# Kernel tuning notes

Measured on AMD Instinct MI355X. Metric: run time of the kernel, lower is better.

The kernel has to match this reference:

```python
import jax, jax.numpy as jnp
import numpy as np

# Dims: B INRs, N probe points, d_in=2 coords, hidden H, out D_OUT, proj P
B, N, D_IN, H, D_OUT, P = 128, 4096, 2, 128, 3, 128
W0_SIREN = 30.0  # SIREN frequency scale
LN_EPS = 1e-5


def setup_inputs() -> dict:
    key = jax.random.key(0)
    ks = jax.random.split(key, 12)
    sn = lambda k, shape, sc: (jax.random.normal(k, shape, dtype=jnp.float32) * sc)
    return {
        # per-sample SIREN params, torch layout: weight [b, in, out, 1], bias [b, out, 1]
        "w0": sn(ks[0], (B, D_IN, H, 1), 1.0 / D_IN),
        "w1": sn(ks[1], (B, H, H, 1), np.sqrt(6.0 / H) / W0_SIREN),
        "w2": sn(ks[2], (B, H, D_OUT, 1), np.sqrt(6.0 / H) / W0_SIREN),
        "b0": sn(ks[3], (B, H, 1), 0.1),
        "b1": sn(ks[4], (B, H, 1), 0.1),
        "b2": sn(ks[5], (B, D_OUT, 1), 0.1),
        # learned probe coordinates, initialized U[-1, 1) as in the module
        "inputs": jax.random.uniform(ks[6], (1, N, D_IN), dtype=jnp.float32, minval=-1.0, maxval=1.0),
        # projection (num_inputs -> proj_dim) + LayerNorm params, one per probed layer (4 total)
        "pw": sn(ks[7], (4, N, P), 1.0 / np.sqrt(N)),
        "pb": jnp.zeros((4, P), jnp.float32),
        "ln_g": jnp.ones((4, P), jnp.float32),
        "ln_b": jnp.zeros((4, P), jnp.float32),
    }


def _layernorm(x, g, b):
    m = jnp.mean(x, axis=-1, keepdims=True)
    v = jnp.mean(jnp.square(x - m), axis=-1, keepdims=True)
    return (x - m) * jax.lax.rsqrt(v + LN_EPS) * g + b


def reference(w0, w1, w2, b0, b1, b2, inputs, pw, pb, ln_g, ln_b):
    b = w0.shape[0]
    x = jnp.broadcast_to(inputs, (b,) + inputs.shape[1:])  # [b, n, d_in]

    def lin(h, W, bb):
        # per-sample linear: [b,n,i] @ [b,i,o] + [b,1,o]
        return jnp.einsum('bni,bio->bno', h, W[..., 0]) + bb[:, None, :, 0]

    h1 = jnp.sin(W0_SIREN * lin(x, w0, b0))   # [b, n, H]
    h2 = jnp.sin(W0_SIREN * lin(h1, w1, b1))  # [b, n, H]
    h3 = lin(h2, w2, b2)                      # [b, n, D_OUT] (last layer: no sine)
    feats = [x, h1, h2, h3]  # probe features per node layer (input coords + activations)

    outs = []
    for i, f in enumerate(feats):
        # permute to [b, dim_i, n], project n -> P, then LayerNorm over P
        z = jnp.einsum('bnd,np->bdp', f, pw[i]) + pb[i]
        outs.append(_layernorm(z, ln_g[i], ln_b[i]))
    return jnp.concatenate(outs, axis=1)  # [b, d_in + H + H + D_OUT, P]
```

## Files before the change

### kernel.cpp

```cpp
#include <hip/hip_runtime.h>
#include <hip/hip_bf16.h>


typedef unsigned short u16;
typedef __attribute__((ext_vector_type(8))) short short8;
typedef __attribute__((ext_vector_type(4))) short short4v;
typedef __attribute__((ext_vector_type(4))) float f32x4;
typedef __attribute__((ext_vector_type(4))) float float4v;

#define DEV __device__ __forceinline__

#define KSC 4.7746482927568605f

DEV float b2f(u16 h){ return __uint_as_float(((unsigned)h) << 16); }
DEV u16 f2b(float f){
  unsigned u = __float_as_uint(f);
  return (u16)((u + 0x7FFFu + ((u >> 16) & 1u)) >> 16);
}
DEV u16 f2b_hw(float f){
  __hip_bfloat16 h = __float2bfloat16(f);
  return __builtin_bit_cast(unsigned short, h);
}
DEV float sin_rev(float r){
#if __has_builtin(__builtin_amdgcn_sinf)
  return __builtin_amdgcn_sinf(r);
#else
  return __sinf(r * 6.283185307179586f);
#endif
}
template<int C> DEV float dpp_add(float x){
  int yi = __builtin_amdgcn_update_dpp(0, __float_as_int(x), C, 0xF, 0xF, true);
  return x + __int_as_float(yi);
}
DEV float sum16(float x){
  x = dpp_add<0x128>(x); x = dpp_add<0x124>(x);
  x = dpp_add<0x122>(x); x = dpp_add<0x121>(x);
  return x;
}

DEV int is_bf16_fmt(const void* lng){ return *(const unsigned*)lng == 0x3F803F80u; }
struct In {
  const float* f; const u16* h; int bf;
  DEV In(const void* p, int b_) : f((const float*)p), h((const u16*)p), bf(b_) {}
  DEV float at(size_t i) const { return bf ? b2f(h[i]) : f[i]; }
};

__global__ __launch_bounds__(256) void k_prep(const void* pwv, const void* inpv,
                                              const void* lngv,
                                              u16* __restrict__ pwT,
                                              float* __restrict__ xbuf,
                                              float* __restrict__ zpart){
  const int bf = is_bf16_fmt(lngv);
  const int t = threadIdx.x;
  if (blockIdx.x == 256){
    In inp(inpv, bf);
    for (int i = t; i < 8192; i += 256) xbuf[i] = inp.at(i);
    return;
  }
  In pw(pwv, bf);
  const int layer = blockIdx.x >> 6;
  const int nc = blockIdx.x & 63;
  const int n0 = nc * 64;

  if (layer == 0){
    In inp(inpv, bf);
    const int d = t >> 7, p = t & 127;
    float s = 0.f;
#pragma unroll 8
    for (int k = 0; k < 64; k++)
      s = fmaf(inp.at((size_t)(n0 + k) * 2 + d),
               pw.at((size_t)(n0 + k) * 128 + p), s);
    zpart[(size_t)nc * 384 + d * 128 + p] = s;
    return;
  }

  __shared__ u16 tile[64 * 129];
  const size_t base = ((size_t)layer * 4096 + n0) * 128;
#pragma unroll
  for (int k = 0; k < 32; k++){
    int idx = k * 256 + t, n = idx >> 7, p = idx & 127;
    tile[n * 129 + p] = f2b(pw.at(base + (size_t)n * 128 + p));
  }
  if (layer == 3 && t < 128){
    float s = 0.f;
#pragma unroll 8
    for (int k = 0; k < 64; k++)
      s += pw.at(base + (size_t)k * 128 + t);
    zpart[(size_t)nc * 384 + 256 + t] = s;
  }
  __syncthreads();
  u16* dst = pwT + (size_t)layer * 128 * 4096 + n0;
#pragma unroll
  for (int k = 0; k < 32; k++){
    int idx = k * 256 + t, p = idx >> 6, n = idx & 63;
    dst[(size_t)p * 4096 + n] = tile[n * 129 + p];
  }
}

__global__ __launch_bounds__(384)
void k_zs2(const float* __restrict__ zpart, float* __restrict__ zs){
  const int t = threadIdx.x;
  float s = 0.f;
  for (int c = 0; c < 64; c++) s += zpart[(size_t)c * 384 + t];
  zs[t] = s;
}

#define S_NK 136
#define S_T  40

template<bool PARTIAL>
__global__ __launch_bounds__(512, 2)
void k_main(const void* w0v, const void* w1v, const void* w2v,
            const void* b0v, const void* b1v, const void* b2v,
            const void* pbv, const void* lgv, const void* lbv,
            const u16* __restrict__ pwTg, const float* __restrict__ xbuf,
            const float* __restrict__ zs,
            float* __restrict__ outp, int TS){
  __shared__ __align__(16) u16 spw1[128 * S_T];
  __shared__ __align__(16) u16 spw23[2][2][128 * S_T];
  __shared__ __align__(16) u16 sh1nk[32 * S_NK];
  __shared__ __align__(16) u16 sh1T[128 * S_T];
  __shared__ __align__(16) u16 sh2T[2][128 * S_T];
  __shared__ float sW2[512];
  __shared__ float sb2[4];
  __shared__ float sPB[512], sG[512], sBB[512];

  float* sP1 = (float*)sh1nk;
  float* sP2 = (float*)sh1T;
  float* sM  = (float*)sh2T;
  float* sI  = (float*)sh2T + 512;

  const int bf = is_bf16_fmt(lgv);
  In w0(w0v, bf), w1(w1v, bf), w2(w2v, bf), b0(b0v, bf), b1(b1v, bf),
     b2(b2v, bf), pb(pbv, bf), lg(lgv, bf), lb(lbv, bf);

  const int t = threadIdx.x;
  const int b = blockIdx.x & 127, sseg = blockIdx.x >> 7;
  const int lane = t & 63, wave = t >> 6, quad = lane >> 4, r16 = lane & 15;
  const int oo = wave * 16 + r16;

  if (t >= 256 && t < 384){
    int i = t - 256;
    sW2[i * 4 + 0] = w2.at(((size_t)b * 128 + i) * 3 + 0);
    sW2[i * 4 + 1] = w2.at(((size_t)b * 128 + i) * 3 + 1);
    sW2[i * 4 + 2] = w2.at(((size_t)b * 128 + i) * 3 + 2);
    sW2[i * 4 + 3] = 0.f;
  }
  if (t < 4) sb2[t] = (t < 3) ? b2.at(b * 3 + t) : 0.f;
  sPB[t] = pb.at(t); sG[t] = lg.at(t); sBB[t] = lb.at(t);

  const int p1n = t >> 4, p1hb = (t & 15) * 8;
  float w00[8], w01[8], b00[8];
#pragma unroll
  for (int j = 0; j < 8; j++){
    w00[j] = w0.at((size_t)b * 256 + p1hb + j) * KSC;
    w01[j] = w0.at((size_t)b * 256 + 128 + p1hb + j) * KSC;
    b00[j] = b0.at((size_t)b * 128 + p1hb + j) * KSC;
  }
  const int p2h = t & 127, p2nb = (t >> 7) * 8;
  const float q00 = w0.at((size_t)b * 256 + p2h) * KSC;
  const float q01 = w0.at((size_t)b * 256 + 128 + p2h) * KSC;
  const float qb0 = b0.at((size_t)b * 128 + p2h) * KSC;
  const float bias1k = b1.at((size_t)b * 128 + oo) * KSC;

  short8 w1f[4];
#pragma unroll
  for (int ks = 0; ks < 4; ks++){
#pragma unroll
    for (int j = 0; j < 8; j++)
      w1f[ks][j] = (short)f2b(w1.at((size_t)b * 16384 +
                                    (size_t)(ks * 32 + quad * 8 + j) * 128 + oo));
  }

  const int pwrow = t >> 2, pwc = t & 3;
  const u16* pwsrc = pwTg + (size_t)524288 + (size_t)pwrow * 4096 + pwc * 8;
  const int pwdofs = pwrow * S_T + pwc * 8;
  const int bofs = oo * S_T + quad * 8;

  const f32x4 zz = {0.f,0.f,0.f,0.f};
  f32x4 az1[8], az2[8], ay[8];
#pragma unroll
  for (int i = 0; i < 8; i++){ az1[i] = zz; az2[i] = zz; ay[i] = zz; }

  const int n0first = sseg * TS * 32;
  short8 pwv[3];
#pragma unroll
  for (int L = 0; L < 3; L++)
    pwv[L] = *(const short8*)(pwsrc + (size_t)L * 524288 + n0first);
  float2 xp1 = *(const float2*)(xbuf + (size_t)(n0first + p1n) * 2);

  __syncthreads();

  int cb = 0;
  for (int nt = 0; nt < TS; nt++){
    const int n0 = (sseg * TS + nt) * 32;

    float4v xq[4];
#pragma unroll
    for (int q = 0; q < 4; q++)
      xq[q] = *(const float4v*)(xbuf + (size_t)(n0 + p2nb) * 2 + q * 4);
    *(short8*)&spw1[pwdofs] = pwv[0];
    *(short8*)&spw23[cb][0][pwdofs] = pwv[1];
    *(short8*)&spw23[cb][1][pwdofs] = pwv[2];
    {
      short8 v;
#pragma unroll
      for (int j = 0; j < 8; j++){
        float a = fmaf(xp1.y, w01[j], fmaf(xp1.x, w00[j], b00[j]));
        a -= rintf(a);
        v[j] = (short)f2b_hw(sin_rev(a));
      }
      *(short8*)&sh1nk[p1n * S_NK + p1hb] = v;
    }
    {
      short8 v;
#pragma unroll
      for (int j = 0; j < 8; j++){
        float x0 = xq[j >> 1][(j & 1) * 2], x1 = xq[j >> 1][(j & 1) * 2 + 1];
        float a = fmaf(x1, q01, fmaf(x0, q00, qb0));
        a -= rintf(a);
        v[j] = (short)f2b_hw(sin_rev(a));
      }
      *(short8*)&sh1T[p2h * S_T + p2nb] = v;
    }
    if (nt){
      const u16* s2p  = sh2T[cb ^ 1];
      const short8 bb2 = *(const short8*)&spw23[cb ^ 1][0][bofs];
      const short8 bb3 = *(const short8*)&spw23[cb ^ 1][1][bofs];
#pragma unroll
      for (int mb = 0; mb < 8; mb++){
        short8 a = *(const short8*)&s2p[(mb * 16 + r16) * S_T + quad * 8];
        az2[mb] = __builtin_amdgcn_mfma_f32_16x16x32_bf16(a, bb2, az2[mb], 0, 0, 0);
        ay[mb]  = __builtin_amdgcn_mfma_f32_16x16x32_bf16(a, bb3, ay[mb], 0, 0, 0);
      }
    }
    __syncthreads();

    {
      const int nn = (nt + 1 < TS) ? nt + 1 : nt;
      const int n0n = (sseg * TS + nn) * 32;
      short8 pwn[3];
#pragma unroll
      for (int L = 0; L < 3; L++)
        pwn[L] = *(const short8*)(pwsrc + (size_t)L * 524288 + n0n);
      float2 xp1n = *(const float2*)(xbuf + (size_t)(n0n + p1n) * 2);

      f32x4 h0 = zz, h1a = zz;
#pragma unroll
      for (int ks = 0; ks < 4; ks++){
        h0  = __builtin_amdgcn_mfma_f32_16x16x32_bf16(
                *(short8*)&sh1nk[r16 * S_NK + ks * 32 + quad * 8], w1f[ks], h0, 0, 0, 0);
        h1a = __builtin_amdgcn_mfma_f32_16x16x32_bf16(
                *(short8*)&sh1nk[(16 + r16) * S_NK + ks * 32 + quad * 8], w1f[ks], h1a, 0, 0, 0);
      }
#pragma unroll
      for (int mb = 0; mb < 8; mb++)
        az1[mb] = __builtin_amdgcn_mfma_f32_16x16x32_bf16(
                    *(short8*)&sh1T[(mb * 16 + r16) * S_T + quad * 8],
                    *(short8*)&spw1[bofs], az1[mb], 0, 0, 0);
      {
        short4v v;
#pragma unroll
        for (int r = 0; r < 4; r++){
          float a = fmaf(h0[r], KSC, bias1k); a -= rintf(a);
          v[r] = (short)f2b_hw(sin_rev(a));
        }
        *(short4v*)&sh2T[cb][oo * S_T + quad * 4] = v;
#pragma unroll
        for (int r = 0; r < 4; r++){
          float a = fmaf(h1a[r], KSC, bias1k); a -= rintf(a);
          v[r] = (short)f2b_hw(sin_rev(a));
        }
        *(short4v*)&sh2T[cb][oo * S_T + 16 + quad * 4] = v;
      }

#pragma unroll
      for (int L = 0; L < 3; L++) pwv[L] = pwn[L];
      xp1 = xp1n;
    }
    __syncthreads();
    cb ^= 1;
  }

  {
    const u16* s2p  = sh2T[cb ^ 1];
    const short8 bb2 = *(const short8*)&spw23[cb ^ 1][0][bofs];
    const short8 bb3 = *(const short8*)&spw23[cb ^ 1][1][bofs];
#pragma unroll
    for (int mb = 0; mb < 8; mb++){
      short8 a = *(const short8*)&s2p[(mb * 16 + r16) * S_T + quad * 8];
      az2[mb] = __builtin_amdgcn_mfma_f32_16x16x32_bf16(a, bb2, az2[mb], 0, 0, 0);
      ay[mb]  = __builtin_amdgcn_mfma_f32_16x16x32_bf16(a, bb3, ay[mb], 0, 0, 0);
    }
  }

  const int p = oo;
  float z3v[3];
#pragma unroll
  for (int d = 0; d < 3; d++){
    float a = 0.f;
#pragma unroll
    for (int mb = 0; mb < 8; mb++)
#pragma unroll
      for (int r = 0; r < 4; r++)
        a = fmaf(sW2[(mb * 16 + quad * 4 + r) * 4 + d], ay[mb][r], a);
    a += __shfl_xor(a, 16, 64); a += __shfl_xor(a, 32, 64);
    z3v[d] = a;
  }
  if (!PARTIAL){
    const float S3v = zs[256 + p];
#pragma unroll
    for (int d = 0; d < 3; d++) z3v[d] += sb2[d] * S3v;
  }

  if (PARTIAL){
    float* zp = outp + ((size_t)(sseg * 128 + b)) * 261 * 128;
    if (quad == 0){
#pragma unroll
      for (int d = 0; d < 3; d++) zp[(size_t)(258 + d) * 128 + p] = z3v[d];
    }
#pragma unroll
    for (int mb = 0; mb < 8; mb++)
#pragma unroll
      for (int r = 0; r < 4; r++){
        int drow = mb * 16 + quad * 4 + r;
        zp[(size_t)(2 + drow) * 128 + p]   = az1[mb][r];
        zp[(size_t)(130 + drow) * 128 + p] = az2[mb][r];
      }
    return;
  }

  const float pb0v = sPB[p],       pb1v = sPB[128 + p];
  const float pb2v = sPB[256 + p], pb3v = sPB[384 + p];

  auto rowsum = [&](float v, int row, bool wr){
    float s1 = sum16(v), s2 = sum16(v * v);
    if (wr && r16 == 0){ sP1[row * 8 + wave] = s1; sP2[row * 8 + wave] = s2; }
  };
#pragma unroll
  for (int mb = 0; mb < 8; mb++)
#pragma unroll
    for (int r = 0; r < 4; r++)
      rowsum(az1[mb][r] + pb1v, 2 + mb * 16 + quad * 4 + r, true);
#pragma unroll
  for (int mb = 0; mb < 8; mb++)
#pragma unroll
    for (int r = 0; r < 4; r++)
      rowsum(az2[mb][r] + pb2v, 130 + mb * 16 + quad * 4 + r, true);
#pragma unroll
  for (int d = 0; d < 3; d++) rowsum(z3v[d] + pb3v, 258 + d, quad == 0);
  __syncthreads();

  if (t < 2){
    float s1 = 0.f, s2 = 0.f;
    for (int pp = 0; pp < 128; pp++){
      float v = zs[t * 128 + pp] + sPB[pp];
      s1 += v; s2 += v * v;
    }
    float m = s1 * (1.f / 128.f);
    float var = fmaf(-m, m, s2 * (1.f / 128.f));
    sM[t] = m;
    sI[t] = rsqrtf(fmaxf(var, 0.f) + 1e-5f);
  } else if (t < 261){
    float s1 = 0.f, s2 = 0.f;
#pragma unroll
    for (int w = 0; w < 8; w++){ s1 += sP1[t * 8 + w]; s2 += sP2[t * 8 + w]; }
    float m = s1 * (1.f / 128.f);
    float var = fmaf(-m, m, s2 * (1.f / 128.f));
    sM[t] = m;
    sI[t] = rsqrtf(fmaxf(var, 0.f) + 1e-5f);
  }
  __syncthreads();

  const size_t ob = (size_t)b * 261 * 128;
  auto emit = [&](float v, int row, int grp){
    outp[ob + (size_t)row * 128 + p] =
      (v - sM[row]) * sI[row] * sG[grp * 128 + p] + sBB[grp * 128 + p];
  };
  if (quad == 0){
#pragma unroll
    for (int r = 0; r < 2; r++) emit(zs[r * 128 + p] + pb0v, r, 0);
#pragma unroll
    for (int d = 0; d < 3; d++) emit(z3v[d] + pb3v, 258 + d, 3);
  }
#pragma unroll
  for (int mb = 0; mb < 8; mb++)
#pragma unroll
    for (int r = 0; r < 4; r++)
      emit(az1[mb][r] + pb1v, 2 + mb * 16 + quad * 4 + r, 1);
#pragma unroll
  for (int mb = 0; mb < 8; mb++)
#pragma unroll
    for (int r = 0; r < 4; r++)
      emit(az2[mb][r] + pb2v, 130 + mb * 16 + quad * 4 + r, 2);
}

__global__ __launch_bounds__(256)
void k_ln(const float* __restrict__ zp, const void* pbv, const void* lgv,
          const void* lbv, const void* b2v, const float* __restrict__ zs,
          float* __restrict__ out, int split){
  const int bf = is_bf16_fmt(lgv);
  In pb(pbv, bf), lg(lgv, bf), lb(lbv, bf), b2(b2v, bf);
  const int lane = threadIdx.x & 63;
  const int row = blockIdx.x * 4 + (threadIdx.x >> 6);
  const int b = row / 261, d = row % 261;
  const int grp = (d < 2) ? 0 : (d < 130) ? 1 : (d < 258) ? 2 : 3;
  const int p0 = lane * 2;
  float v0 = pb.at(grp * 128 + p0), v1 = pb.at(grp * 128 + p0 + 1);
  if (d < 2){
    v0 += zs[d * 128 + p0];
    v1 += zs[d * 128 + p0 + 1];
  } else {
    for (int s2 = 0; s2 < split; s2++){
      const float* zr = zp + ((size_t)(s2 * 128 + b) * 261 + d) * 128;
      v0 += zr[p0]; v1 += zr[p0 + 1];
    }
    if (d >= 258){
      float bb = b2.at((size_t)b * 3 + (d - 258));
      v0 = fmaf(bb, zs[256 + p0], v0);
      v1 = fmaf(bb, zs[256 + p0 + 1], v1);
    }
  }
  float s1 = v0 + v1, s2s = v0 * v0 + v1 * v1;
#pragma unroll
  for (int o = 1; o < 64; o <<= 1){
    s1 += __shfl_xor(s1, o, 64);
    s2s += __shfl_xor(s2s, o, 64);
  }
  float m = s1 * (1.f / 128.f);
  float var = fmaf(-m, m, s2s * (1.f / 128.f));
  float inv = rsqrtf(fmaxf(var, 0.f) + 1e-5f);
  float2 o2;
  o2.x = (v0 - m) * inv * lg.at(grp * 128 + p0)     + lb.at(grp * 128 + p0);
  o2.y = (v1 - m) * inv * lg.at(grp * 128 + p0 + 1) + lb.at(grp * 128 + p0 + 1);
  *(float2*)(out + (size_t)row * 128 + p0) = o2;
}

extern "C" void kernel_launch(void* const* d_in, const int* in_sizes, int n_in,
                              void* d_out, int out_size, void* d_ws, size_t ws_size,
                              hipStream_t stream){
  const void* w0  = d_in[0];
  const void* w1  = d_in[1];
  const void* w2  = d_in[2];
  const void* b0  = d_in[3];
  const void* b1  = d_in[4];
  const void* b2  = d_in[5];
  const void* inp = d_in[6];
  const void* pw  = d_in[7];
  const void* pb  = d_in[8];
  const void* lng = d_in[9];
  const void* lnb = d_in[10];
  float* out = (float*)d_out;

  char* ws = (char*)d_ws;
  u16* pwT     = (u16*)ws;
  float* xbuf  = (float*)(ws + 4194304);
  float* zs    = (float*)(ws + 4194304 + 32768);
  float* zpart = (float*)(ws + 4194304 + 32768 + 2048);
  const size_t zoff = 4194304 + 32768 + 2048 + 98304;
  float* zp = (float*)(ws + zoff);
  const size_t seg = (size_t)128 * 261 * 128 * 4;

  const int split = (ws_size >= zoff + 2 * seg) ? 2 : 1;

  k_prep<<<257, 256, 0, stream>>>(pw, inp, lng, pwT, xbuf, zpart);
  k_zs2<<<1, 384, 0, stream>>>(zpart, zs);
  if (split == 2){
    k_main<true><<<256, 512, 0, stream>>>(w0, w1, w2, b0, b1, b2,
        pb, lng, lnb, pwT, xbuf, zs, zp, 64);
    k_ln<<<(128 * 261) / 4, 256, 0, stream>>>(zp, pb, lng, lnb, b2, zs, out, 2);
  } else {
    k_main<false><<<128, 512, 0, stream>>>(w0, w1, w2, b0, b1, b2,
        pb, lng, lnb, pwT, xbuf, zs, out, 128);
  }
}
```

Baseline: 228.8 us.

## Fuse split-K reduction and LayerNorm into main kernel via last-block atomic counter

Drops the separate k_ln launch and, in the split path, the k_zs2 launch. Each of the two blocks per sample writes its partial projection, then bumps a per-sample atomic counter, and the second block to arrive sums both partials, reduces zpart into shared memory and applies LayerNorm directly into the output. This removes two kernel launches and the extra pass over the partial buffer, at the cost of a serial tail on the winning block and 64-way zpart reduction repeated per sample. Counters are reset in k_prep each call.

```diff
diff --git a/kernel.cpp b/kernel.cpp
--- a/kernel.cpp
+++ b/kernel.cpp
@@ -49,12 +49,14 @@
                                               const void* lngv,
                                               u16* __restrict__ pwT,
                                               float* __restrict__ xbuf,
-                                              float* __restrict__ zpart){
+                                              float* __restrict__ zpart,
+                                              int* __restrict__ ctr){
   const int bf = is_bf16_fmt(lngv);
   const int t = threadIdx.x;
   if (blockIdx.x == 256){
     In inp(inpv, bf);
     for (int i = t; i < 8192; i += 256) xbuf[i] = inp.at(i);
+    if (t < 128) ctr[t] = 0;
     return;
   }
   In pw(pwv, bf);
@@ -114,8 +116,9 @@
             const void* b0v, const void* b1v, const void* b2v,
             const void* pbv, const void* lgv, const void* lbv,
             const u16* __restrict__ pwTg, const float* __restrict__ xbuf,
-            const float* __restrict__ zs,
-            float* __restrict__ outp, int TS){
+            const float* __restrict__ zs, const float* __restrict__ zpart,
+            int* __restrict__ ctr, float* __restrict__ outp,
+            float* __restrict__ finalout, int TS){
   __shared__ __align__(16) u16 spw1[128 * S_T];
   __shared__ __align__(16) u16 spw23[2][2][128 * S_T];
   __shared__ __align__(16) u16 sh1nk[32 * S_NK];
@@ -124,11 +127,13 @@
   __shared__ float sW2[512];
   __shared__ float sb2[4];
   __shared__ float sPB[512], sG[512], sBB[512];
+  __shared__ int sWin;
 
   float* sP1 = (float*)sh1nk;
   float* sP2 = (float*)sh1T;
   float* sM  = (float*)sh2T;
   float* sI  = (float*)sh2T + 512;
+  float* szs = (float*)sh1nk;
 
   const int bf = is_bf16_fmt(lgv);
   In w0(w0v, bf), w1(w1v, bf), w2(w2v, bf), b0(b0v, bf), b1(b1v, bf),
@@ -314,19 +319,69 @@
   }
 
   if (PARTIAL){
-    float* zp = outp + ((size_t)(sseg * 128 + b)) * 261 * 128;
+    float* zpb = outp + ((size_t)(sseg * 128 + b)) * 261 * 128;
     if (quad == 0){
 #pragma unroll
-      for (int d = 0; d < 3; d++) zp[(size_t)(258 + d) * 128 + p] = z3v[d];
+      for (int d = 0; d < 3; d++) zpb[(size_t)(258 + d) * 128 + p] = z3v[d];
     }
 #pragma unroll
     for (int mb = 0; mb < 8; mb++)
 #pragma unroll
       for (int r = 0; r < 4; r++){
         int drow = mb * 16 + quad * 4 + r;
-        zp[(size_t)(2 + drow) * 128 + p]   = az1[mb][r];
-        zp[(size_t)(130 + drow) * 128 + p] = az2[mb][r];
-      }
+        zpb[(size_t)(2 + drow) * 128 + p]   = az1[mb][r];
+        zpb[(size_t)(130 + drow) * 128 + p] = az2[mb][r];
+      }
+
+    __threadfence();
+    __syncthreads();
+    if (t == 0)
+      sWin = __hip_atomic_fetch_add(&ctr[b], 1, __ATOMIC_ACQ_REL,
+                                    __HIP_MEMORY_SCOPE_AGENT);
+    __syncthreads();
+    if (sWin != 1) return;
+    __threadfence();
+
+    for (int i = t; i < 384; i += 512){
+      float s = 0.f;
+      for (int c = 0; c < 64; c++) s += zpart[(size_t)c * 384 + i];
+      szs[i] = s;
+    }
+    __syncthreads();
+
+    const float* z0p = outp + (size_t)b * 261 * 128;
+    const float* z1p = outp + (size_t)(128 + b) * 261 * 128;
+    float* og = finalout + (size_t)b * 261 * 128;
+    const int p0 = lane * 2;
+    for (int d = wave; d < 261; d += 8){
+      const int grp = (d < 2) ? 0 : (d < 130) ? 1 : (d < 258) ? 2 : 3;
+      float v0 = sPB[grp * 128 + p0], v1 = sPB[grp * 128 + p0 + 1];
+      if (d < 2){
+        v0 += szs[d * 128 + p0];
+        v1 += szs[d * 128 + p0 + 1];
+      } else {
+        v0 += z0p[(size_t)d * 128 + p0]; v1 += z0p[(size_t)d * 128 + p0 + 1];
+        v0 += z1p[(size_t)d * 128 + p0]; v1 += z1p[(size_t)d * 128 + p0 + 1];
+        if (d >= 258){
+          float bb = sb2[d - 258];
+          v0 = fmaf(bb, szs[256 + p0], v0);
+          v1 = fmaf(bb, szs[256 + p0 + 1], v1);
+        }
+      }
+      float s1 = v0 + v1, s2s = v0 * v0 + v1 * v1;
+#pragma unroll
+      for (int o = 1; o < 64; o <<= 1){
+        s1 += __shfl_xor(s1, o, 64);
+        s2s += __shfl_xor(s2s, o, 64);
+      }
+      float m = s1 * (1.f / 128.f);
+      float var = fmaf(-m, m, s2s * (1.f / 128.f));
+      float inv = rsqrtf(fmaxf(var, 0.f) + 1e-5f);
+      float2 o2;
+      o2.x = (v0 - m) * inv * sG[grp * 128 + p0]     + sBB[grp * 128 + p0];
+      o2.y = (v1 - m) * inv * sG[grp * 128 + p0 + 1] + sBB[grp * 128 + p0 + 1];
+      *(float2*)(og + (size_t)d * 128 + p0) = o2;
+    }
     return;
   }
 
@@ -393,47 +448,6 @@
 #pragma unroll
     for (int r = 0; r < 4; r++)
       emit(az2[mb][r] + pb2v, 130 + mb * 16 + quad * 4 + r, 2);
-}
-
-__global__ __launch_bounds__(256)
-void k_ln(const float* __restrict__ zp, const void* pbv, const void* lgv,
-          const void* lbv, const void* b2v, const float* __restrict__ zs,
-          float* __restrict__ out, int split){
-  const int bf = is_bf16_fmt(lgv);
-  In pb(pbv, bf), lg(lgv, bf), lb(lbv, bf), b2(b2v, bf);
-  const int lane = threadIdx.x & 63;
-  const int row = blockIdx.x * 4 + (threadIdx.x >> 6);
-  const int b = row / 261, d = row % 261;
-  const int grp = (d < 2) ? 0 : (d < 130) ? 1 : (d < 258) ? 2 : 3;
-  const int p0 = lane * 2;
-  float v0 = pb.at(grp * 128 + p0), v1 = pb.at(grp * 128 + p0 + 1);
-  if (d < 2){
-    v0 += zs[d * 128 + p0];
-    v1 += zs[d * 128 + p0 + 1];
-  } else {
-    for (int s2 = 0; s2 < split; s2++){
-      const float* zr = zp + ((size_t)(s2 * 128 + b) * 261 + d) * 128;
-      v0 += zr[p0]; v1 += zr[p0 + 1];
-    }
-    if (d >= 258){
-      float bb = b2.at((size_t)b * 3 + (d - 258));
-      v0 = fmaf(bb, zs[256 + p0], v0);
-      v1 = fmaf(bb, zs[256 + p0 + 1], v1);
-    }
-  }
-  float s1 = v0 + v1, s2s = v0 * v0 + v1 * v1;
-#pragma unroll
-  for (int o = 1; o < 64; o <<= 1){
-    s1 += __shfl_xor(s1, o, 64);
-    s2s += __shfl_xor(s2s, o, 64);
-  }
-  float m = s1 * (1.f / 128.f);
-  float var = fmaf(-m, m, s2s * (1.f / 128.f));
-  float inv = rsqrtf(fmaxf(var, 0.f) + 1e-5f);
-  float2 o2;
-  o2.x = (v0 - m) * inv * lg.at(grp * 128 + p0)     + lb.at(grp * 128 + p0);
-  o2.y = (v1 - m) * inv * lg.at(grp * 128 + p0 + 1) + lb.at(grp * 128 + p0 + 1);
-  *(float2*)(out + (size_t)row * 128 + p0) = o2;
 }
 
 extern "C" void kernel_launch(void* const* d_in, const int* in_sizes, int n_in,
@@ -457,20 +471,20 @@
   float* xbuf  = (float*)(ws + 4194304);
   float* zs    = (float*)(ws + 4194304 + 32768);
   float* zpart = (float*)(ws + 4194304 + 32768 + 2048);
-  const size_t zoff = 4194304 + 32768 + 2048 + 98304;
+  int*   ctr   = (int*)  (ws + 4194304 + 32768 + 2048 + 98304);
+  const size_t zoff = 4194304 + 32768 + 2048 + 98304 + 512;
   float* zp = (float*)(ws + zoff);
   const size_t seg = (size_t)128 * 261 * 128 * 4;
 
   const int split = (ws_size >= zoff + 2 * seg) ? 2 : 1;
 
-  k_prep<<<257, 256, 0, stream>>>(pw, inp, lng, pwT, xbuf, zpart);
-  k_zs2<<<1, 384, 0, stream>>>(zpart, zs);
+  k_prep<<<257, 256, 0, stream>>>(pw, inp, lng, pwT, xbuf, zpart, ctr);
   if (split == 2){
     k_main<true><<<256, 512, 0, stream>>>(w0, w1, w2, b0, b1, b2,
-        pb, lng, lnb, pwT, xbuf, zs, zp, 64);
-    k_ln<<<(128 * 261) / 4, 256, 0, stream>>>(zp, pb, lng, lnb, b2, zs, out, 2);
+        pb, lng, lnb, pwT, xbuf, zs, zpart, ctr, zp, out, 64);
   } else {
+    k_zs2<<<1, 384, 0, stream>>>(zpart, zs);
     k_main<false><<<128, 512, 0, stream>>>(w0, w1, w2, b0, b1, b2,
-        pb, lng, lnb, pwT, xbuf, zs, out, 128);
-  }
-}
+        pb, lng, lnb, pwT, xbuf, zs, zpart, ctr, out, out, 128);
+  }
+}
```

Result: slower. 313.9 us (+37.2%).

## Pre-swizzle projection weights into MFMA fragment layout and load B operands directly to registers

Applied to the files above, without the earlier changes.

The prep kernel now writes the transposed projection weights in a per-fragment layout that matches the MFMA B-operand order, using one contiguous 4096-element block per 32-row chunk. The main kernel loads each lane's B fragment straight from global memory into registers. This removes the shared-memory staging buffers for the projection weights, their stores, and the LDS reads. It also shrinks LDS use and the workspace, but every lane now issues its own global loads and the layer-2/3 fragments need extra registers to stay in flight across the software pipeline.

```diff
diff --git a/kernel.cpp b/kernel.cpp
--- a/kernel.cpp
+++ b/kernel.cpp
@@ -47,7 +47,7 @@
 
 __global__ __launch_bounds__(256) void k_prep(const void* pwv, const void* inpv,
                                               const void* lngv,
-                                              u16* __restrict__ pwT,
+                                              u16* __restrict__ pwT2,
                                               float* __restrict__ xbuf,
                                               float* __restrict__ zpart){
   const int bf = is_bf16_fmt(lngv);
@@ -89,11 +89,14 @@
     zpart[(size_t)nc * 384 + 256 + t] = s;
   }
   __syncthreads();
-  u16* dst = pwT + (size_t)layer * 128 * 4096 + n0;
+  u16* dst = pwT2 + ((size_t)(layer - 1) * 128 + nc * 2) * 4096;
 #pragma unroll
   for (int k = 0; k < 32; k++){
-    int idx = k * 256 + t, p = idx >> 6, n = idx & 63;
-    dst[(size_t)p * 4096 + n] = tile[n * 129 + p];
+    int o = k * 256 + t;
+    int frag = (o >> 3) & 511, j = o & 7;
+    int p = ((frag >> 6) << 4) | ((frag >> 2) & 15);
+    int nn = ((o >> 12) << 5) | ((frag & 3) << 3) | j;
+    dst[o] = tile[nn * 129 + p];
   }
 }
 
@@ -116,8 +119,6 @@
             const u16* __restrict__ pwTg, const float* __restrict__ xbuf,
             const float* __restrict__ zs,
             float* __restrict__ outp, int TS){
-  __shared__ __align__(16) u16 spw1[128 * S_T];
-  __shared__ __align__(16) u16 spw23[2][2][128 * S_T];
   __shared__ __align__(16) u16 sh1nk[32 * S_NK];
   __shared__ __align__(16) u16 sh1T[128 * S_T];
   __shared__ __align__(16) u16 sh2T[2][128 * S_T];
@@ -172,22 +173,21 @@
                                     (size_t)(ks * 32 + quad * 8 + j) * 128 + oo));
   }
 
-  const int pwrow = t >> 2, pwc = t & 3;
-  const u16* pwsrc = pwTg + (size_t)524288 + (size_t)pwrow * 4096 + pwc * 8;
-  const int pwdofs = pwrow * S_T + pwc * 8;
-  const int bofs = oo * S_T + quad * 8;
+  const int frag = wave * 64 + r16 * 4 + quad;
+  const u16* bsrc = pwTg + (size_t)frag * 8;
 
   const f32x4 zz = {0.f,0.f,0.f,0.f};
   f32x4 az1[8], az2[8], ay[8];
 #pragma unroll
   for (int i = 0; i < 8; i++){ az1[i] = zz; az2[i] = zz; ay[i] = zz; }
 
-  const int n0first = sseg * TS * 32;
-  short8 pwv[3];
+  const int nb0 = sseg * TS;
+  short8 bbc[3];
 #pragma unroll
   for (int L = 0; L < 3; L++)
-    pwv[L] = *(const short8*)(pwsrc + (size_t)L * 524288 + n0first);
-  float2 xp1 = *(const float2*)(xbuf + (size_t)(n0first + p1n) * 2);
+    bbc[L] = *(const short8*)(bsrc + ((size_t)L * 128 + nb0) * 4096);
+  short8 bb2p = bbc[1], bb3p = bbc[2];
+  float2 xp1 = *(const float2*)(xbuf + (size_t)(nb0 * 32 + p1n) * 2);
 
   __syncthreads();
 
@@ -199,9 +199,6 @@
 #pragma unroll
     for (int q = 0; q < 4; q++)
       xq[q] = *(const float4v*)(xbuf + (size_t)(n0 + p2nb) * 2 + q * 4);
-    *(short8*)&spw1[pwdofs] = pwv[0];
-    *(short8*)&spw23[cb][0][pwdofs] = pwv[1];
-    *(short8*)&spw23[cb][1][pwdofs] = pwv[2];
     {
       short8 v;
 #pragma unroll
@@ -224,26 +221,24 @@
       *(short8*)&sh1T[p2h * S_T + p2nb] = v;
     }
     if (nt){
-      const u16* s2p  = sh2T[cb ^ 1];
-      const short8 bb2 = *(const short8*)&spw23[cb ^ 1][0][bofs];
-      const short8 bb3 = *(const short8*)&spw23[cb ^ 1][1][bofs];
+      const u16* s2p = sh2T[cb ^ 1];
 #pragma unroll
       for (int mb = 0; mb < 8; mb++){
         short8 a = *(const short8*)&s2p[(mb * 16 + r16) * S_T + quad * 8];
-        az2[mb] = __builtin_amdgcn_mfma_f32_16x16x32_bf16(a, bb2, az2[mb], 0, 0, 0);
-        ay[mb]  = __builtin_amdgcn_mfma_f32_16x16x32_bf16(a, bb3, ay[mb], 0, 0, 0);
+        az2[mb] = __builtin_amdgcn_mfma_f32_16x16x32_bf16(a, bb2p, az2[mb], 0, 0, 0);
+        ay[mb]  = __builtin_amdgcn_mfma_f32_16x16x32_bf16(a, bb3p, ay[mb], 0, 0, 0);
       }
     }
     __syncthreads();
 
     {
       const int nn = (nt + 1 < TS) ? nt + 1 : nt;
-      const int n0n = (sseg * TS + nn) * 32;
-      short8 pwn[3];
+      const int nbn = sseg * TS + nn;
+      short8 bbn[3];
 #pragma unroll
       for (int L = 0; L < 3; L++)
-        pwn[L] = *(const short8*)(pwsrc + (size_t)L * 524288 + n0n);
-      float2 xp1n = *(const float2*)(xbuf + (size_t)(n0n + p1n) * 2);
+        bbn[L] = *(const short8*)(bsrc + ((size_t)L * 128 + nbn) * 4096);
+      float2 xp1n = *(const float2*)(xbuf + (size_t)(nbn * 32 + p1n) * 2);
 
       f32x4 h0 = zz, h1a = zz;
 #pragma unroll
@@ -257,7 +252,7 @@
       for (int mb = 0; mb < 8; mb++)
         az1[mb] = __builtin_amdgcn_mfma_f32_16x16x32_bf16(
                     *(short8*)&sh1T[(mb * 16 + r16) * S_T + quad * 8],
-                    *(short8*)&spw1[bofs], az1[mb], 0, 0, 0);
+                    bbc[0], az1[mb], 0, 0, 0);
       {
         short4v v;
 #pragma unroll
@@ -274,8 +269,9 @@
         *(short4v*)&sh2T[cb][oo * S_T + 16 + quad * 4] = v;
       }
 
-#pragma unroll
-      for (int L = 0; L < 3; L++) pwv[L] = pwn[L];
+      bb2p = bbc[1]; bb3p = bbc[2];
+#pragma unroll
+      for (int L = 0; L < 3; L++) bbc[L] = bbn[L];
       xp1 = xp1n;
     }
     __syncthreads();
@@ -283,14 +279,12 @@
   }
 
   {
-    const u16* s2p  = sh2T[cb ^ 1];
-    const short8 bb2 = *(const short8*)&spw23[cb ^ 1][0][bofs];
-    const short8 bb3 = *(const short8*)&spw23[cb ^ 1][1][bofs];
+    const u16* s2p = sh2T[cb ^ 1];
 #pragma unroll
     for (int mb = 0; mb < 8; mb++){
       short8 a = *(const short8*)&s2p[(mb * 16 + r16) * S_T + quad * 8];
-      az2[mb] = __builtin_amdgcn_mfma_f32_16x16x32_bf16(a, bb2, az2[mb], 0, 0, 0);
-      ay[mb]  = __builtin_amdgcn_mfma_f32_16x16x32_bf16(a, bb3, ay[mb], 0, 0, 0);
+      az2[mb] = __builtin_amdgcn_mfma_f32_16x16x32_bf16(a, bb2p, az2[mb], 0, 0, 0);
+      ay[mb]  = __builtin_amdgcn_mfma_f32_16x16x32_bf16(a, bb3p, ay[mb], 0, 0, 0);
     }
   }
 
@@ -453,24 +447,24 @@
   float* out = (float*)d_out;
 
   char* ws = (char*)d_ws;
-  u16* pwT     = (u16*)ws;
-  float* xbuf  = (float*)(ws + 4194304);
-  float* zs    = (float*)(ws + 4194304 + 32768);
-  float* zpart = (float*)(ws + 4194304 + 32768 + 2048);
-  const size_t zoff = 4194304 + 32768 + 2048 + 98304;
+  u16* pwT2    = (u16*)ws;
+  float* xbuf  = (float*)(ws + 3145728);
+  float* zs    = (float*)(ws + 3145728 + 32768);
+  float* zpart = (float*)(ws + 3145728 + 32768 + 2048);
+  const size_t zoff = 3145728 + 32768 + 2048 + 98304;
   float* zp = (float*)(ws + zoff);
   const size_t seg = (size_t)128 * 261 * 128 * 4;
 
   const int split = (ws_size >= zoff + 2 * seg) ? 2 : 1;
 
-  k_prep<<<257, 256, 0, stream>>>(pw, inp, lng, pwT, xbuf, zpart);
+  k_prep<<<257, 256, 0, stream>>>(pw, inp, lng, pwT2, xbuf, zpart);
   k_zs2<<<1, 384, 0, stream>>>(zpart, zs);
   if (split == 2){
     k_main<true><<<256, 512, 0, stream>>>(w0, w1, w2, b0, b1, b2,
-        pb, lng, lnb, pwT, xbuf, zs, zp, 64);
+        pb, lng, lnb, pwT2, xbuf, zs, zp, 64);
     k_ln<<<(128 * 261) / 4, 256, 0, stream>>>(zp, pb, lng, lnb, b2, zs, out, 2);
   } else {
     k_main<false><<<128, 512, 0, stream>>>(w0, w1, w2, b0, b1, b2,
-        pb, lng, lnb, pwT, xbuf, zs, out, 128);
-  }
-}
+        pb, lng, lnb, pwT2, xbuf, zs, out, 128);
+  }
+}
```

New measurement: 221.1 us. 1.03x faster.
